# Kernel optimization log

Measured on AMD Instinct MI355X. Metric: run time of the kernel, lower is better.

Reference implementation:

```python
import jax, jax.numpy as jnp
import numpy as np


def _apply1(state, w, m00, m01, m10, m11):
    # state: (N,16) complex64; apply 2x2 gate on wire w (wire 0 = most significant bit)
    st = state.reshape(-1, 2 ** w, 2, 2 ** (3 - w))
    a, b = st[:, :, 0, :], st[:, :, 1, :]
    def bc(v):
        return jnp.reshape(jnp.asarray(v, state.dtype), (-1, 1, 1))
    na = bc(m00) * a + bc(m01) * b
    nb = bc(m10) * a + bc(m11) * b
    return jnp.stack([na, nb], axis=2).reshape(-1, 16)


def _ry(state, theta, w):
    c, s = jnp.cos(theta / 2), jnp.sin(theta / 2)
    return _apply1(state, w, c, -s, s, c)


def _rx(state, theta, w):
    c, s = jnp.cos(theta / 2), jnp.sin(theta / 2)
    return _apply1(state, w, c, -1j * s, -1j * s, c)


def _rz(state, theta, w):
    e = jnp.exp(-0.5j * theta.astype(jnp.complex64))
    return _apply1(state, w, e, 0.0, 0.0, jnp.conj(e))


def _cnot(state, ctrl, tgt):
    s = state.reshape((-1, 2, 2, 2, 2))
    c_ax, t_ax = ctrl + 1, tgt + 1
    s0 = jnp.take(s, 0, axis=c_ax)
    s1 = jnp.take(s, 1, axis=c_ax)
    t2 = t_ax - (1 if t_ax > c_ax else 0)
    s1 = jnp.flip(s1, axis=t2)
    return jnp.stack([s0, s1], axis=c_ax).reshape(-1, 16)


def _measure_z(state):
    # expval of PauliZ on each wire: (N,4)
    p = (state.real ** 2 + state.imag ** 2).reshape(-1, 2, 2, 2, 2)
    z = jnp.array([1.0, -1.0], p.dtype)
    exps = []
    for w in range(4):
        axes = tuple(a for a in (1, 2, 3, 4) if a != w + 1)
        exps.append(p.sum(axes) @ z)
    return jnp.stack(exps, axis=1)


def setup_inputs() -> dict:
    key = jax.random.key(0)
    k = jax.random.split(key, 6)
    B = 2048
    x = jax.random.uniform(k[0], (B, 1, 28, 28), dtype=jnp.float32)
    emb_W = jax.random.normal(k[1], (4, 4), dtype=jnp.float32) * 0.5
    emb_b = jnp.zeros((4,), jnp.float32)
    q_params = jax.random.uniform(k[2], (5,), dtype=jnp.float32, minval=0.0, maxval=2.0 * np.pi)
    lin_W = jax.random.normal(k[3], (10, 784), dtype=jnp.float32) * (1.0 / np.sqrt(784.0))
    lin_b = jnp.zeros((10,), jnp.float32)
    return {"x": x, "emb_W": emb_W, "emb_b": emb_b, "q_params": q_params, "lin_W": lin_W, "lin_b": lin_b}


def reference(x, emb_W, emb_b, q_params, lin_W, lin_b):
    B = x.shape[0]
    img = x.reshape(B, 28, 28)
    # 2x2 non-overlapping patches, row-major over (r, c), ordered [tl, tr, bl, br]
    patches = img.reshape(B, 14, 2, 14, 2).transpose(0, 1, 3, 2, 4).reshape(B, 196, 4)
    ang = (patches @ emb_W.T + emb_b).reshape(-1, 4)  # (B*196, 4)
    N = ang.shape[0]
    state = jnp.zeros((N, 16), jnp.complex64).at[:, 0].set(1.0)
    # data encoding: RY(angle_i) on wire i
    for w in range(4):
        state = _ry(state, ang[:, w], w)
    # fixed 8-op random layer (learnable scalar rotation params + CNOT entanglers)
    state = _rx(state, q_params[0], 0)
    state = _ry(state, q_params[1], 1)
    state = _rz(state, q_params[2], 2)
    state = _cnot(state, 0, 1)
    state = _rx(state, q_params[3], 3)
    state = _cnot(state, 2, 3)
    state = _ry(state, q_params[4], 2)
    state = _cnot(state, 1, 2)
    feats = _measure_z(state).reshape(B, 196 * 4)  # patch-major concat, 4 expvals each
    logits = feats @ lin_W.T + lin_b
    return jax.nn.log_softmax(logits, axis=-1)
```

## Files before the change

### kernel.cpp

```cpp
#include <hip/hip_runtime.h>
#include <hip/hip_bf16.h>


template<int STRIDE>
__device__ __forceinline__ void ry_gate(float re[16], float im[16], float c, float s) {
    #pragma unroll
    for (int base = 0; base < 16; base += 2 * STRIDE) {
        #pragma unroll
        for (int off = 0; off < STRIDE; ++off) {
            const int i0 = base + off, i1 = i0 + STRIDE;
            const float r0 = re[i0], m0 = im[i0], r1 = re[i1], m1 = im[i1];
            re[i0] = c * r0 - s * r1;  im[i0] = c * m0 - s * m1;
            re[i1] = s * r0 + c * r1;  im[i1] = s * m0 + c * m1;
        }
    }
}

template<int STRIDE>
__device__ __forceinline__ void rx_gate(float re[16], float im[16], float c, float s) {
    #pragma unroll
    for (int base = 0; base < 16; base += 2 * STRIDE) {
        #pragma unroll
        for (int off = 0; off < STRIDE; ++off) {
            const int i0 = base + off, i1 = i0 + STRIDE;
            const float r0 = re[i0], m0 = im[i0], r1 = re[i1], m1 = im[i1];
            re[i0] = c * r0 + s * m1;  im[i0] = c * m0 - s * r1;
            re[i1] = s * m0 + c * r1;  im[i1] = -s * r0 + c * m1;
        }
    }
}

template<int STRIDE>
__device__ __forceinline__ void rz_gate(float re[16], float im[16], float c, float s) {
    #pragma unroll
    for (int base = 0; base < 16; base += 2 * STRIDE) {
        #pragma unroll
        for (int off = 0; off < STRIDE; ++off) {
            const int i0 = base + off, i1 = i0 + STRIDE;
            const float r0 = re[i0], m0 = im[i0], r1 = re[i1], m1 = im[i1];
            re[i0] = c * r0 + s * m0;  im[i0] = c * m0 - s * r0;
            re[i1] = c * r1 - s * m1;  im[i1] = s * r1 + c * m1;
        }
    }
}

template<int CMASK, int TMASK>
__device__ __forceinline__ void cnot_gate(float re[16], float im[16]) {
    #pragma unroll
    for (int i = 0; i < 16; ++i) {
        if ((i & CMASK) && !(i & TMASK)) {
            const int j = i | TMASK;
            float t;
            t = re[i]; re[i] = re[j]; re[j] = t;
            t = im[i]; im[i] = im[j]; im[j] = t;
        }
    }
}

__global__ __launch_bounds__(256) void quanv_fused(
    const float* __restrict__ x,
    const float* __restrict__ embW,
    const float* __restrict__ embB,
    const float* __restrict__ qp,
    const float* __restrict__ linW,
    const float* __restrict__ linB,
    float* __restrict__ out)
{
    const int b   = blockIdx.x;
    const int tid = threadIdx.x;

    __shared__ float simg[784];
    __shared__ float sred[4][10];

    const float* img = x + (size_t)b * 784;
    #pragma unroll
    for (int i = 0; i < 4; ++i) {
        const int idx = tid + 256 * i;
        if (idx < 784) simg[idx] = img[idx];
    }
    __syncthreads();

    float part[10];
    #pragma unroll
    for (int c = 0; c < 10; ++c) part[c] = 0.0f;

    if (tid < 196) {
        const int pi = tid / 14, pj = tid % 14;
        const float p0 = simg[(2 * pi) * 28 + 2 * pj];
        const float p1 = simg[(2 * pi) * 28 + 2 * pj + 1];
        const float p2 = simg[(2 * pi + 1) * 28 + 2 * pj];
        const float p3 = simg[(2 * pi + 1) * 28 + 2 * pj + 1];

        float cA[4], sA[4];
        #pragma unroll
        for (int w = 0; w < 4; ++w) {
            const float a = embB[w] + embW[4 * w + 0] * p0 + embW[4 * w + 1] * p1
                                    + embW[4 * w + 2] * p2 + embW[4 * w + 3] * p3;
            __sincosf(0.5f * a, &sA[w], &cA[w]);
        }

        float qc[5], qs[5];
        #pragma unroll
        for (int i = 0; i < 5; ++i) __sincosf(0.5f * qp[i], &qs[i], &qc[i]);

        float re[16], im[16];
        #pragma unroll
        for (int idx = 0; idx < 16; ++idx) {
            float v = 1.0f;
            #pragma unroll
            for (int w = 0; w < 4; ++w)
                v *= ((idx >> (3 - w)) & 1) ? sA[w] : cA[w];
            re[idx] = v;
            im[idx] = 0.0f;
        }

        rx_gate<8>(re, im, qc[0], qs[0]);
        ry_gate<4>(re, im, qc[1], qs[1]);
        rz_gate<2>(re, im, qc[2], qs[2]);
        cnot_gate<8, 4>(re, im);
        rx_gate<1>(re, im, qc[3], qs[3]);
        cnot_gate<2, 1>(re, im);
        ry_gate<2>(re, im, qc[4], qs[4]);
        cnot_gate<4, 2>(re, im);

        float p[16];
        #pragma unroll
        for (int i = 0; i < 16; ++i) p[i] = re[i] * re[i] + im[i] * im[i];
        float f[4];
        #pragma unroll
        for (int w = 0; w < 4; ++w) {
            const int mask = 8 >> w;
            float acc = 0.0f;
            #pragma unroll
            for (int i = 0; i < 16; ++i) acc += (i & mask) ? -p[i] : p[i];
            f[w] = acc;
        }

        #pragma unroll
        for (int c = 0; c < 10; ++c) {
            const float4 wv = *reinterpret_cast<const float4*>(linW + c * 784 + tid * 4);
            part[c] = f[0] * wv.x + f[1] * wv.y + f[2] * wv.z + f[3] * wv.w;
        }
    }

    #pragma unroll
    for (int c = 0; c < 10; ++c) {
        part[c] += __shfl_down(part[c], 32);
        part[c] += __shfl_down(part[c], 16);
        part[c] += __shfl_down(part[c], 8);
        part[c] += __shfl_down(part[c], 4);
        part[c] += __shfl_down(part[c], 2);
        part[c] += __shfl_down(part[c], 1);
    }
    const int lane = tid & 63;
    const int wv   = tid >> 6;
    if (lane == 0) {
        #pragma unroll
        for (int c = 0; c < 10; ++c) sred[wv][c] = part[c];
    }
    __syncthreads();

    if (tid == 0) {
        float logit[10];
        float m = -1e30f;
        #pragma unroll
        for (int c = 0; c < 10; ++c) {
            logit[c] = sred[0][c] + sred[1][c] + sred[2][c] + sred[3][c] + linB[c];
            m = fmaxf(m, logit[c]);
        }
        float ssum = 0.0f;
        #pragma unroll
        for (int c = 0; c < 10; ++c) ssum += expf(logit[c] - m);
        const float lse = m + logf(ssum);
        #pragma unroll
        for (int c = 0; c < 10; ++c) out[(size_t)b * 10 + c] = logit[c] - lse;
    }
}

extern "C" void kernel_launch(void* const* d_in, const int* in_sizes, int n_in,
                              void* d_out, int out_size, void* d_ws, size_t ws_size,
                              hipStream_t stream) {
    const float* x    = (const float*)d_in[0];
    const float* embW = (const float*)d_in[1];
    const float* embB = (const float*)d_in[2];
    const float* qp   = (const float*)d_in[3];
    const float* linW = (const float*)d_in[4];
    const float* linB = (const float*)d_in[5];
    float* out = (float*)d_out;

    const int B = in_sizes[0] / 784;
    quanv_fused<<<B, 256, 0, stream>>>(x, embW, embB, qp, linW, linB, out);
}
```

Measured before the change: 75.43 us.

## Load patches directly from global, factor state init, parallelize log-softmax

Drops the shared-memory image staging and its barrier; each thread now reads its 2x2 patch straight from global memory with two float2 loads. The product-state initialisation is factored into shared partial products, the Z expectations are computed with a butterfly-style reduction, and the final log-softmax is spread over 16 lanes using shuffles instead of running on a single thread. This removes a block-wide sync and some redundant arithmetic, at the cost of less-coalesced, strided global loads.

```diff
diff --git a/kernel.cpp b/kernel.cpp
--- a/kernel.cpp
+++ b/kernel.cpp
@@ -69,27 +69,18 @@
     const int b   = blockIdx.x;
     const int tid = threadIdx.x;
 
-    __shared__ float simg[784];
     __shared__ float sred[4][10];
-
-    const float* img = x + (size_t)b * 784;
-    #pragma unroll
-    for (int i = 0; i < 4; ++i) {
-        const int idx = tid + 256 * i;
-        if (idx < 784) simg[idx] = img[idx];
-    }
-    __syncthreads();
 
     float part[10];
     #pragma unroll
     for (int c = 0; c < 10; ++c) part[c] = 0.0f;
 
     if (tid < 196) {
-        const int pi = tid / 14, pj = tid % 14;
-        const float p0 = simg[(2 * pi) * 28 + 2 * pj];
-        const float p1 = simg[(2 * pi) * 28 + 2 * pj + 1];
-        const float p2 = simg[(2 * pi + 1) * 28 + 2 * pj];
-        const float p3 = simg[(2 * pi + 1) * 28 + 2 * pj + 1];
+        const unsigned pi = (unsigned)tid / 14u, pj = (unsigned)tid % 14u;
+        const float* img = x + (size_t)b * 784;
+        const float2 r0 = *reinterpret_cast<const float2*>(img + (2 * pi) * 28 + 2 * pj);
+        const float2 r1 = *reinterpret_cast<const float2*>(img + (2 * pi + 1) * 28 + 2 * pj);
+        const float p0 = r0.x, p1 = r0.y, p2 = r1.x, p3 = r1.y;
 
         float cA[4], sA[4];
         #pragma unroll
@@ -104,14 +95,19 @@
         for (int i = 0; i < 5; ++i) __sincosf(0.5f * qp[i], &qs[i], &qc[i]);
 
         float re[16], im[16];
+        float ab[4], abc[8];
+        ab[0] = cA[0] * cA[1];  ab[1] = cA[0] * sA[1];
+        ab[2] = sA[0] * cA[1];  ab[3] = sA[0] * sA[1];
         #pragma unroll
-        for (int idx = 0; idx < 16; ++idx) {
-            float v = 1.0f;
-            #pragma unroll
-            for (int w = 0; w < 4; ++w)
-                v *= ((idx >> (3 - w)) & 1) ? sA[w] : cA[w];
-            re[idx] = v;
-            im[idx] = 0.0f;
+        for (int j = 0; j < 4; ++j) {
+            abc[2 * j]     = ab[j] * cA[2];
+            abc[2 * j + 1] = ab[j] * sA[2];
+        }
+        #pragma unroll
+        for (int k = 0; k < 8; ++k) {
+            re[2 * k]     = abc[k] * cA[3];
+            re[2 * k + 1] = abc[k] * sA[3];
+            im[2 * k] = 0.0f;  im[2 * k + 1] = 0.0f;
         }
 
         rx_gate<8>(re, im, qc[0], qs[0]);
@@ -126,20 +122,21 @@
         float p[16];
         #pragma unroll
         for (int i = 0; i < 16; ++i) p[i] = re[i] * re[i] + im[i] * im[i];
-        float f[4];
+
+        float a8[8], a4[4], a2[2];
+        float f0 = 0.0f, f1 = 0.0f, f2 = 0.0f;
         #pragma unroll
-        for (int w = 0; w < 4; ++w) {
-            const int mask = 8 >> w;
-            float acc = 0.0f;
-            #pragma unroll
-            for (int i = 0; i < 16; ++i) acc += (i & mask) ? -p[i] : p[i];
-            f[w] = acc;
-        }
+        for (int j = 0; j < 8; ++j) { a8[j] = p[j] + p[j + 8]; f0 += p[j] - p[j + 8]; }
+        #pragma unroll
+        for (int j = 0; j < 4; ++j) { a4[j] = a8[j] + a8[j + 4]; f1 += a8[j] - a8[j + 4]; }
+        #pragma unroll
+        for (int j = 0; j < 2; ++j) { a2[j] = a4[j] + a4[j + 2]; f2 += a4[j] - a4[j + 2]; }
+        const float f3 = a2[0] - a2[1];
 
         #pragma unroll
         for (int c = 0; c < 10; ++c) {
             const float4 wv = *reinterpret_cast<const float4*>(linW + c * 784 + tid * 4);
-            part[c] = f[0] * wv.x + f[1] * wv.y + f[2] * wv.z + f[3] * wv.w;
+            part[c] = f0 * wv.x + f1 * wv.y + f2 * wv.z + f3 * wv.w;
         }
     }
 
@@ -160,20 +157,22 @@
     }
     __syncthreads();
 
-    if (tid == 0) {
-        float logit[10];
-        float m = -1e30f;
-        #pragma unroll
-        for (int c = 0; c < 10; ++c) {
-            logit[c] = sred[0][c] + sred[1][c] + sred[2][c] + sred[3][c] + linB[c];
-            m = fmaxf(m, logit[c]);
-        }
-        float ssum = 0.0f;
-        #pragma unroll
-        for (int c = 0; c < 10; ++c) ssum += expf(logit[c] - m);
-        const float lse = m + logf(ssum);
-        #pragma unroll
-        for (int c = 0; c < 10; ++c) out[(size_t)b * 10 + c] = logit[c] - lse;
+    if (tid < 16) {
+        float logit = -1e30f;
+        if (tid < 10)
+            logit = sred[0][tid] + sred[1][tid] + sred[2][tid] + sred[3][tid] + linB[tid];
+        float m = logit;
+        m = fmaxf(m, __shfl_xor(m, 1, 16));
+        m = fmaxf(m, __shfl_xor(m, 2, 16));
+        m = fmaxf(m, __shfl_xor(m, 4, 16));
+        m = fmaxf(m, __shfl_xor(m, 8, 16));
+        float e = (tid < 10) ? expf(logit - m) : 0.0f;
+        e += __shfl_xor(e, 1, 16);
+        e += __shfl_xor(e, 2, 16);
+        e += __shfl_xor(e, 4, 16);
+        e += __shfl_xor(e, 8, 16);
+        const float lse = m + logf(e);
+        if (tid < 10) out[(size_t)b * 10 + tid] = logit - lse;
     }
 }
 
```

After: 74.82 us. About the same (-0.8%).
